# Optimization experiments

Hardware: AMD Instinct MI355X
Metric: run time of the kernel (lower is better)

Reference implementation:

```python
import jax, jax.numpy as jnp
import numpy as np

EMB = 1024
HEADS = 8
NUM_REL = 5
BS = 8
SLEN = 1024


def setup_inputs() -> dict:
    key = jax.random.key(0)
    ks = jax.random.split(key, 11)

    def lin(k, out_dim, in_dim):
        k1, k2 = jax.random.split(k)
        w = 0.02 * jax.random.normal(k1, (out_dim, in_dim), dtype=jnp.float32)
        b = 0.02 * jax.random.normal(k2, (out_dim,), dtype=jnp.float32)
        return w, b

    p = {}
    for i, pref in enumerate(["nq", "nk", "nv", "no", "tq", "tk", "tv", "to"]):
        w, b = lin(ks[i], EMB, EMB)
        p[pref + "_w"] = w
        p[pref + "_b"] = b
    tp_w, tp_b = lin(ks[8], NUM_REL, EMB)
    h_in = jax.random.normal(ks[9], (BS, SLEN, EMB), dtype=jnp.float32)
    word_mask = jnp.ones((BS, SLEN), dtype=bool)
    return {"h_in": h_in, "word_mask": word_mask, **p, "tp_w": tp_w, "tp_b": tp_b}


def _mha(x, mask, qw, qb, kw, kb, vw, vb, ow, ob):
    # Self-attention with key-padding mask; returns (output, attn_weights).
    bs, slen, dim = x.shape
    dh = dim // HEADS

    def split(t):  # [bs, slen, dim] -> [bs, h, slen, dh]
        return t.reshape(bs, slen, HEADS, dh).transpose(0, 2, 1, 3)

    q = split(x @ qw.T + qb) / jnp.sqrt(jnp.asarray(dh, x.dtype))
    k = split(x @ kw.T + kb)
    v = split(x @ vw.T + vb)
    scores = jnp.einsum('bhqd,bhkd->bhqk', q, k)
    scores = jnp.where(mask[:, None, None, :], scores, jnp.asarray(-1e9, x.dtype))
    w = jax.nn.softmax(scores, axis=-1)  # [bs, h, slen, slen]
    ctx = jnp.einsum('bhqk,bhkd->bhqd', w, v).transpose(0, 2, 1, 3).reshape(bs, slen, dim)
    return ctx @ ow.T + ob, w


def reference(h_in, word_mask, nq_w, nq_b, nk_w, nk_b, nv_w, nv_b, no_w, no_b,
              tq_w, tq_b, tk_w, tk_b, tv_w, tv_b, to_w, to_b, tp_w, tp_b):
    # Edge norms: sum attention weights over heads, then symmetrize.
    _, norm_w = _mha(h_in, word_mask, nq_w, nq_b, nk_w, nk_b, nv_w, nv_b, no_w, no_b)
    norm_w = norm_w.sum(axis=1)  # edge_norm_agg == 'sum' -> [bs, slen, slen]
    norms = norm_w + norm_w.transpose(0, 2, 1)

    # Edge types: second attention, project to relation logits, pairwise outer-sum.
    type_out, _ = _mha(h_in, word_mask, tq_w, tq_b, tk_w, tk_b, tv_w, tv_b, to_w, to_b)
    logits = type_out @ tp_w.T + tp_b  # [bs, slen, R]
    pair = logits[:, :, None, :] + logits[:, None, :, :]  # [bs, slen, slen, R]
    type_probs = jax.nn.softmax(pair, axis=-1)  # log_softmax(...).exp()
    return norms, type_probs
```

## Files before the change

kernel.cpp:

```cpp
#include <hip/hip_runtime.h>

using u16 = unsigned short;
typedef __bf16 bf16x8 __attribute__((ext_vector_type(8)));
typedef float  f32x4  __attribute__((ext_vector_type(4)));

__device__ __forceinline__ float b2f(u16 u){
  union { unsigned int i; float f; } v; v.i = ((unsigned int)u) << 16; return v.f;
}
__device__ __forceinline__ u16 f2b(float f){
  union { float f; unsigned int i; } v; v.f = f;
  unsigned int r = v.i + 0x7FFFu + ((v.i >> 16) & 1u);
  return (u16)(r >> 16);
}
__device__ __forceinline__ float waveMax(float v){
  #pragma unroll
  for (int o = 32; o > 0; o >>= 1) v = fmaxf(v, __shfl_xor(v, o, 64));
  return v;
}
__device__ __forceinline__ float waveSum(float v){
  #pragma unroll
  for (int o = 32; o > 0; o >>= 1) v += __shfl_xor(v, o, 64);
  return v;
}
__device__ __forceinline__ void async_cp16(const u16* g, u16* l){
  __builtin_amdgcn_global_load_lds((const __attribute__((address_space(1))) void*)g,
                                   (__attribute__((address_space(3))) void*)l, 16, 0, 0);
}

__global__ __launch_bounds__(256)
void cvt_f2b4(const float* __restrict__ s, u16* __restrict__ d, long long n4)
{
  long long i = (long long)blockIdx.x * 256 + threadIdx.x;
  long long st = (long long)gridDim.x * 256;
  for (; i < n4; i += st) {
    float4 v = ((const float4*)s)[i];
    ushort4 o; o.x = f2b(v.x); o.y = f2b(v.y); o.z = f2b(v.z); o.w = f2b(v.w);
    ((ushort4*)d)[i] = o;
  }
}

__global__ __launch_bounds__(256)
void bcat_k(const float* b0, const float* b1, const float* b2, const float* b3,
            const float* b4, float* __restrict__ dst)
{
  int t = blockIdx.x * 256 + threadIdx.x;
  const float* s = (t < 1024) ? b0 : (t < 2048) ? b1 : (t < 3072) ? b2 : (t < 4096) ? b3 : b4;
  dst[t] = s[t & 1023];
}

__global__ __launch_bounds__(256)
void fuse_w(const float* __restrict__ tow, const float* __restrict__ tob,
            const float* __restrict__ tpw, const float* __restrict__ tpb,
            float* __restrict__ Wc, float* __restrict__ bc)
{
  int t = blockIdx.x * 256 + threadIdx.x;
  int r = t >> 10, c = t & 1023;
  float acc = 0.f;
  for (int k = 0; k < 1024; k++) acc += tpw[r * 1024 + k] * tow[k * 1024 + c];
  Wc[t] = acc;
  if (t < 5) {
    float a = 0.f;
    for (int k = 0; k < 1024; k++) a += tpw[t * 1024 + k] * tob[k];
    bc[t] = a + tpb[t];
  }
}

template<int HAS_BIAS>
__global__ __launch_bounds__(256)
void gemm_bt(const u16* __restrict__ A, const u16* __restrict__ B,
             u16* __restrict__ C, const float* __restrict__ bias,
             int lda, int ldb, int ldc, int K,
             long long sAo, long long sAi, long long sBo, long long sBi,
             long long sCo, long long sCi, int zshift, int zmask, float alpha)
{
  int zo = (int)(blockIdx.z >> zshift), zi = (int)(blockIdx.z & zmask);
  A += zo * sAo + zi * sAi;
  B += zo * sBo + zi * sBi;
  long long coff = zo * sCo + zi * sCi;
  int m0 = blockIdx.y * 128, n0 = blockIdx.x * 128;

  __shared__ alignas(16) u16 sA[128 * 32];
  __shared__ alignas(16) u16 sB[128 * 32];

  int t = threadIdx.x;
  int lane = t & 63, wave = t >> 6;
  int quad = lane >> 4, l16 = lane & 15;
  int wm = (wave >> 1) << 6, wn = (wave & 1) << 6;
  int srow = t >> 2, scg = (t & 3) << 3;
  int wb = wave << 9;

  const u16* ga = A + (long long)(m0 + srow) * lda + scg;
  const u16* gb = B + (long long)(n0 + srow) * ldb + scg;

  f32x4 acc[4][4] = {};

  for (int k0 = 0; k0 < K; k0 += 32) {
    __syncthreads();
    async_cp16(ga + k0,                sA + wb);
    async_cp16(ga + 64ll * lda + k0,   sA + wb + 2048);
    async_cp16(gb + k0,                sB + wb);
    async_cp16(gb + 64ll * ldb + k0,   sB + wb + 2048);
    __syncthreads();

    bf16x8 af[4], bfr[4];
    #pragma unroll
    for (int mi = 0; mi < 4; mi++)
      af[mi] = *(const bf16x8*)(&sA[(wm + mi * 16 + l16) * 32 + quad * 8]);
    #pragma unroll
    for (int ni = 0; ni < 4; ni++)
      bfr[ni] = *(const bf16x8*)(&sB[(wn + ni * 16 + l16) * 32 + quad * 8]);
    #pragma unroll
    for (int mi = 0; mi < 4; mi++)
      #pragma unroll
      for (int ni = 0; ni < 4; ni++)
        acc[mi][ni] = __builtin_amdgcn_mfma_f32_16x16x32_bf16(af[mi], bfr[ni], acc[mi][ni], 0, 0, 0);
  }

  #pragma unroll
  for (int ni = 0; ni < 4; ni++) {
    int n = n0 + wn + ni * 16 + l16;
    float bv = 0.f;
    if (HAS_BIAS) bv = bias[n];
    #pragma unroll
    for (int mi = 0; mi < 4; mi++) {
      int mb = m0 + wm + mi * 16 + quad * 4;
      #pragma unroll
      for (int r = 0; r < 4; r++) {
        float v = alpha * (acc[mi][ni][r] + bv);
        C[coff + (long long)(mb + r) * ldc + n] = f2b(v);
      }
    }
  }
}

__global__ __launch_bounds__(256)
void norm_softmax_sum(const u16* __restrict__ sc, float* __restrict__ out)
{
  int i = blockIdx.x, b = blockIdx.y;
  int t = threadIdx.x;
  int wave = t >> 6;
  __shared__ float wm_[4], wsu[4];
  float acc[4] = {0.f, 0.f, 0.f, 0.f};

  for (int h = 0; h < 8; h++) {
    const u16* row = sc + (((long long)(b * 8 + h)) << 20) + ((long long)i << 10);
    float v[4];
    #pragma unroll
    for (int p = 0; p < 4; p++) v[p] = b2f(row[t + 256 * p]);
    float m = fmaxf(fmaxf(v[0], v[1]), fmaxf(v[2], v[3]));
    m = waveMax(m);
    if ((t & 63) == 0) wm_[wave] = m;
    __syncthreads();
    m = fmaxf(fmaxf(wm_[0], wm_[1]), fmaxf(wm_[2], wm_[3]));
    float e[4], s = 0.f;
    #pragma unroll
    for (int p = 0; p < 4; p++) { e[p] = __expf(v[p] - m); s += e[p]; }
    s = waveSum(s);
    if ((t & 63) == 0) wsu[wave] = s;
    __syncthreads();
    s = wsu[0] + wsu[1] + wsu[2] + wsu[3];
    float inv = 1.f / s;
    #pragma unroll
    for (int p = 0; p < 4; p++) acc[p] += e[p] * inv;
  }
  float* o = out + ((long long)b << 20) + ((long long)i << 10);
  #pragma unroll
  for (int p = 0; p < 4; p++) o[t + 256 * p] = acc[p];
}

__global__ __launch_bounds__(256)
void sym_inplace(float* __restrict__ nw)
{
  int tj = blockIdx.x, ti = blockIdx.y, b = blockIdx.z;
  if (tj < ti) return;
  float* base = nw + ((long long)b << 20);
  __shared__ float sij[64][65], sji[64][65];
  int t = threadIdx.x;
  #pragma unroll
  for (int p = 0; p < 16; p++) {
    int idx = p * 256 + t; int r = idx >> 6, c = idx & 63;
    sij[r][c] = base[(long long)(ti * 64 + r) * 1024 + tj * 64 + c];
    sji[r][c] = base[(long long)(tj * 64 + r) * 1024 + ti * 64 + c];
  }
  __syncthreads();
  #pragma unroll
  for (int p = 0; p < 16; p++) {
    int idx = p * 256 + t; int r = idx >> 6, c = idx & 63;
    base[(long long)(ti * 64 + r) * 1024 + tj * 64 + c] = sij[r][c] + sji[c][r];
    if (ti != tj)
      base[(long long)(tj * 64 + r) * 1024 + ti * 64 + c] = sji[r][c] + sij[c][r];
  }
}

__global__ __launch_bounds__(256)
void w5_k(const u16* __restrict__ proj, const float* __restrict__ Wc,
          float* __restrict__ w5)
{
  int jb = blockIdx.x, bh = blockIdx.y;
  int b = bh >> 3, h = bh & 7;
  int t = threadIdx.x;
  int j = jb * 256 + t;
  __shared__ float sWc[5][128];
  if (t < 128) {
    #pragma unroll
    for (int r = 0; r < 5; r++) sWc[r][t] = Wc[r * 1024 + h * 128 + t];
  }
  __syncthreads();
  const u16* vrow = proj + (long long)(b * 1024 + j) * 5120 + 4096 + h * 128;
  float acc[5] = {0.f, 0.f, 0.f, 0.f, 0.f};
  #pragma unroll
  for (int d0 = 0; d0 < 128; d0 += 8) {
    bf16x8 v = *(const bf16x8*)(vrow + d0);
    #pragma unroll
    for (int q = 0; q < 8; q++) {
      float f = (float)v[q];
      #pragma unroll
      for (int r = 0; r < 5; r++) acc[r] += f * sWc[r][d0 + q];
    }
  }
  #pragma unroll
  for (int r = 0; r < 5; r++) w5[(((long long)(bh * 5 + r)) << 10) + j] = acc[r];
}

__global__ __launch_bounds__(256)
void type_logits(const u16* __restrict__ sc, const float* __restrict__ w5,
                 const float* __restrict__ bc, float* __restrict__ lg)
{
  int b = blockIdx.y;
  int t = threadIdx.x;
  int wave = t >> 6, l = t & 63;
  int i = blockIdx.x * 4 + wave;
  __shared__ float sW5[5120];
  float acc[5] = {0.f, 0.f, 0.f, 0.f, 0.f};

  for (int h = 0; h < 8; h++) {
    const u16* row = sc + (((long long)(b * 8 + h)) << 20) + ((long long)i << 10);
    const float* wb = w5 + ((long long)(b * 8 + h)) * 5120;
    float v[16];
    #pragma unroll
    for (int k = 0; k < 16; k++) v[k] = b2f(row[l + 64 * k]);
    __syncthreads();
    #pragma unroll
    for (int p = 0; p < 20; p++) sW5[p * 256 + t] = wb[p * 256 + t];
    float m = v[0];
    #pragma unroll
    for (int k = 1; k < 16; k++) m = fmaxf(m, v[k]);
    m = waveMax(m);
    float e[16], s = 0.f;
    #pragma unroll
    for (int k = 0; k < 16; k++) { e[k] = __expf(v[k] - m); s += e[k]; }
    s = waveSum(s);
    float inv = 1.f / s;
    __syncthreads();
    #pragma unroll
    for (int r = 0; r < 5; r++) {
      float a = 0.f;
      #pragma unroll
      for (int k = 0; k < 16; k++) a += e[k] * sW5[r * 1024 + l + 64 * k];
      acc[r] += a * inv;
    }
  }
  #pragma unroll
  for (int r = 0; r < 5; r++) acc[r] = waveSum(acc[r]);
  if (l == 0) {
    #pragma unroll
    for (int r = 0; r < 5; r++) lg[(long long)(b * 1024 + i) * 5 + r] = acc[r] + bc[r];
  }
}

__global__ __launch_bounds__(256)
void pairwise_probs(const float* __restrict__ lg, float* __restrict__ out)
{
  int i = blockIdx.x, b = blockIdx.y;
  int t = threadIdx.x;
  __shared__ float sin_[5120];
  __shared__ float sout[5120];
  const float* lb = lg + (long long)b * 5120;
  #pragma unroll
  for (int p = 0; p < 20; p++) sin_[p * 256 + t] = lb[p * 256 + t];
  __syncthreads();
  float li[5];
  #pragma unroll
  for (int r = 0; r < 5; r++) li[r] = sin_[i * 5 + r];
  #pragma unroll
  for (int p = 0; p < 4; p++) {
    int j = t + 256 * p;
    float x[5]; float m = -1e30f;
    #pragma unroll
    for (int r = 0; r < 5; r++) { x[r] = li[r] + sin_[j * 5 + r]; m = fmaxf(m, x[r]); }
    float s = 0.f;
    #pragma unroll
    for (int r = 0; r < 5; r++) { x[r] = __expf(x[r] - m); s += x[r]; }
    float inv = 1.f / s;
    #pragma unroll
    for (int r = 0; r < 5; r++) sout[j * 5 + r] = x[r] * inv;
  }
  __syncthreads();
  float4* ob = (float4*)(out + ((long long)(b * 1024 + i)) * 5120);
  #pragma unroll
  for (int q = 0; q < 5; q++) ob[q * 256 + t] = ((const float4*)sout)[q * 256 + t];
}

extern "C" void kernel_launch(void* const* d_in, const int* in_sizes, int n_in,
                              void* d_out, int out_size, void* d_ws, size_t ws_size,
                              hipStream_t stream)
{
  const float* h_in = (const float*)d_in[0];
  const float* nq_w = (const float*)d_in[2];
  const float* nq_b = (const float*)d_in[3];
  const float* nk_w = (const float*)d_in[4];
  const float* nk_b = (const float*)d_in[5];
  const float* tq_w = (const float*)d_in[10];
  const float* tq_b = (const float*)d_in[11];
  const float* tk_w = (const float*)d_in[12];
  const float* tk_b = (const float*)d_in[13];
  const float* tv_w = (const float*)d_in[14];
  const float* tv_b = (const float*)d_in[15];
  const float* to_w = (const float*)d_in[16];
  const float* to_b = (const float*)d_in[17];
  const float* tp_w = (const float*)d_in[18];
  const float* tp_b = (const float*)d_in[19];

  char* ws = (char*)d_ws;
  u16*  hb   = (u16*)(ws);
  u16*  wcat = (u16*)(ws + (16ll  << 20));
  float* bcat= (float*)(ws + (26ll << 20));
  float* Wc  = (float*)(ws + (26ll << 20) + (512 << 10));
  float* bc  = (float*)(ws + (26ll << 20) + (768 << 10));
  float* lg  = (float*)(ws + (27ll << 20));
  u16*  proj = (u16*)(ws + (28ll  << 20));
  float* w5  = (float*)(ws + (108ll << 20));
  u16*  sc   = (u16*)(ws + (140ll << 20));

  float* out_norms = (float*)d_out;
  float* out_types = (float*)d_out + 8388608ll;

  const float qs = 0.08838834764831845f;
  dim3 blk(256);

  cvt_f2b4<<<dim3(2048), blk, 0, stream>>>(h_in, hb, 2097152ll);
  cvt_f2b4<<<dim3(512),  blk, 0, stream>>>(nq_w, wcat,              262144ll);
  cvt_f2b4<<<dim3(512),  blk, 0, stream>>>(nk_w, wcat + 1048576ll,  262144ll);
  cvt_f2b4<<<dim3(512),  blk, 0, stream>>>(tq_w, wcat + 2097152ll,  262144ll);
  cvt_f2b4<<<dim3(512),  blk, 0, stream>>>(tk_w, wcat + 3145728ll,  262144ll);
  cvt_f2b4<<<dim3(512),  blk, 0, stream>>>(tv_w, wcat + 4194304ll,  262144ll);
  bcat_k<<<dim3(20), blk, 0, stream>>>(nq_b, nk_b, tq_b, tk_b, tv_b, bcat);
  fuse_w<<<dim3(20), blk, 0, stream>>>(to_w, to_b, tp_w, tp_b, Wc, bc);

  gemm_bt<1><<<dim3(40,64,1), blk, 0, stream>>>(hb, wcat, proj, bcat,
      1024,1024,5120,1024, 0,0,0,0,0,0, 0,0, 1.f);

  w5_k<<<dim3(4,64), blk, 0, stream>>>(proj, Wc, w5);

  gemm_bt<0><<<dim3(8,8,64), blk, 0, stream>>>(proj, proj + 1024, sc, nullptr,
      5120,5120,1024,128, 5242880ll,128ll, 5242880ll,128ll, 8388608ll,1048576ll, 3,7, qs);
  norm_softmax_sum<<<dim3(1024,8), blk, 0, stream>>>(sc, out_norms);
  sym_inplace<<<dim3(16,16,8), blk, 0, stream>>>(out_norms);

  gemm_bt<0><<<dim3(8,8,64), blk, 0, stream>>>(proj + 2048, proj + 3072, sc, nullptr,
      5120,5120,1024,128, 5242880ll,128ll, 5242880ll,128ll, 8388608ll,1048576ll, 3,7, qs);
  type_logits<<<dim3(256,8), blk, 0, stream>>>(sc, w5, bc, lg);
  pairwise_probs<<<dim3(1024,8), blk, 0, stream>>>(lg, out_types);
}
```

Before: 741.8 us.

## Fuse norm QK^T with softmax-sum and fold V projection into relation weights

New measurement: 789.5 us. 1.06x slower.

```diff
diff --git a/kernel.cpp b/kernel.cpp
--- a/kernel.cpp
+++ b/kernel.cpp
@@ -41,10 +41,10 @@
 
 __global__ __launch_bounds__(256)
 void bcat_k(const float* b0, const float* b1, const float* b2, const float* b3,
-            const float* b4, float* __restrict__ dst)
+            float* __restrict__ dst)
 {
   int t = blockIdx.x * 256 + threadIdx.x;
-  const float* s = (t < 1024) ? b0 : (t < 2048) ? b1 : (t < 3072) ? b2 : (t < 4096) ? b3 : b4;
+  const float* s = (t < 1024) ? b0 : (t < 2048) ? b1 : (t < 3072) ? b2 : b3;
   dst[t] = s[t & 1023];
 }
 
@@ -65,7 +65,32 @@
   }
 }
 
-template<int HAS_BIAS>
+__global__ __launch_bounds__(256)
+void fuse_wf(const float* __restrict__ tvw, const float* __restrict__ tvb,
+             const float* __restrict__ Wc, u16* __restrict__ WF,
+             float* __restrict__ bias5)
+{
+  int idx = blockIdx.x * 256 + threadIdx.x;
+  int n = idx >> 10, k = idx & 1023;
+  float acc = 0.f;
+  if (n < 40) {
+    int h = n / 5, r = n - h * 5;
+    const float* wcr = Wc + r * 1024 + h * 128;
+    const float* tw = tvw + (h * 128) * 1024 + k;
+    for (int d = 0; d < 128; d++) acc += wcr[d] * tw[d * 1024];
+  }
+  WF[idx] = f2b(acc);
+  if (k == 0) {
+    float a = 0.f;
+    if (n < 40) {
+      int h = n / 5, r = n - h * 5;
+      for (int d = 0; d < 128; d++) a += Wc[r * 1024 + h * 128 + d] * tvb[h * 128 + d];
+    }
+    bias5[n] = a;
+  }
+}
+
+template<int HAS_BIAS, int OUT_F32>
 __global__ __launch_bounds__(256)
 void gemm_bt(const u16* __restrict__ A, const u16* __restrict__ B,
              u16* __restrict__ C, const float* __restrict__ bias,
@@ -127,45 +152,114 @@
       #pragma unroll
       for (int r = 0; r < 4; r++) {
         float v = alpha * (acc[mi][ni][r] + bv);
-        C[coff + (long long)(mb + r) * ldc + n] = f2b(v);
+        if (OUT_F32) ((float*)C)[coff + (long long)(mb + r) * ldc + n] = v;
+        else         C[coff + (long long)(mb + r) * ldc + n] = f2b(v);
       }
     }
   }
 }
 
-__global__ __launch_bounds__(256)
-void norm_softmax_sum(const u16* __restrict__ sc, float* __restrict__ out)
-{
-  int i = blockIdx.x, b = blockIdx.y;
+__global__ __launch_bounds__(512)
+void norm_fused(const u16* __restrict__ proj, float* __restrict__ out)
+{
+  int b = blockIdx.y, i0 = blockIdx.x * 32;
   int t = threadIdx.x;
-  int wave = t >> 6;
-  __shared__ float wm_[4], wsu[4];
-  float acc[4] = {0.f, 0.f, 0.f, 0.f};
+  int lane = t & 63, wave = t >> 6;
+  int quad = lane >> 4, l16 = lane & 15;
+  int wm = (wave >> 2) << 4;
+  int wn = (wave & 3) << 4;
+  int r0 = t >> 4, g = t & 15;
+
+  __shared__ alignas(16) u16 sQ[2][32 * 128];
+  __shared__ alignas(16) u16 sK[2][64 * 128];
+  __shared__ alignas(16) u16 sS[32 * 1044];
+
+  const long long ldp = 4096;
+  const u16* pb = proj + (long long)(b * 1024) * ldp;
+  int srow = t >> 4;
+  int scol = (t & 15) << 3;
+  const float qs = 0.08838834764831845f;
+
+  float acc[16][4];
+  #pragma unroll
+  for (int k = 0; k < 16; k++)
+    #pragma unroll
+    for (int j = 0; j < 4; j++) acc[k][j] = 0.f;
+
+  auto stageQ = [&](int h, int buf){
+    async_cp16(pb + (long long)(i0 + srow) * ldp + h * 128 + scol,
+               &sQ[buf][wave << 9]);
+  };
+  auto stageK = [&](int h, int jt, int buf){
+    const u16* gbase = pb + 1024 + h * 128 + scol;
+    #pragma unroll
+    for (int c = 0; c < 2; c++)
+      async_cp16(gbase + (long long)(jt * 64 + c * 32 + srow) * ldp,
+                 &sK[buf][c * 4096 + (wave << 9)]);
+  };
+
+  int qb = 0, kb = 0;
+  stageQ(0, 0);
+  stageK(0, 0, 0);
+  __syncthreads();
 
   for (int h = 0; h < 8; h++) {
-    const u16* row = sc + (((long long)(b * 8 + h)) << 20) + ((long long)i << 10);
-    float v[4];
-    #pragma unroll
-    for (int p = 0; p < 4; p++) v[p] = b2f(row[t + 256 * p]);
-    float m = fmaxf(fmaxf(v[0], v[1]), fmaxf(v[2], v[3]));
-    m = waveMax(m);
-    if ((t & 63) == 0) wm_[wave] = m;
+    for (int jt = 0; jt < 16; jt++) {
+      if (jt < 15)      stageK(h, jt + 1, kb ^ 1);
+      else if (h < 7) { stageK(h + 1, 0, kb ^ 1); stageQ(h + 1, qb ^ 1); }
+
+      f32x4 accs = {};
+      #pragma unroll
+      for (int kk = 0; kk < 4; kk++) {
+        bf16x8 af  = *(const bf16x8*)(&sQ[qb][(wm + l16) * 128 + kk * 32 + quad * 8]);
+        bf16x8 bf_ = *(const bf16x8*)(&sK[kb][(wn + l16) * 128 + kk * 32 + quad * 8]);
+        accs = __builtin_amdgcn_mfma_f32_16x16x32_bf16(af, bf_, accs, 0, 0, 0);
+      }
+      int jg = jt * 64 + wn + l16;
+      #pragma unroll
+      for (int rr = 0; rr < 4; rr++)
+        sS[(wm + quad * 4 + rr) * 1044 + jg] = f2b(qs * accs[rr]);
+      __syncthreads();
+      kb ^= 1;
+    }
+
+    const u16* sr = sS + r0 * 1044 + g * 4;
+    float m = -1e30f;
+    #pragma unroll
+    for (int k = 0; k < 16; k++) {
+      ushort4 u = *(const ushort4*)(sr + k * 64);
+      m = fmaxf(m, fmaxf(fmaxf(b2f(u.x), b2f(u.y)), fmaxf(b2f(u.z), b2f(u.w))));
+    }
+    #pragma unroll
+    for (int o = 1; o < 16; o <<= 1) m = fmaxf(m, __shfl_xor(m, o, 64));
+    float s = 0.f;
+    #pragma unroll
+    for (int k = 0; k < 16; k++) {
+      ushort4 u = *(const ushort4*)(sr + k * 64);
+      s += __expf(b2f(u.x) - m) + __expf(b2f(u.y) - m)
+         + __expf(b2f(u.z) - m) + __expf(b2f(u.w) - m);
+    }
+    #pragma unroll
+    for (int o = 1; o < 16; o <<= 1) s += __shfl_xor(s, o, 64);
+    float inv = 1.f / s;
+    #pragma unroll
+    for (int k = 0; k < 16; k++) {
+      ushort4 u = *(const ushort4*)(sr + k * 64);
+      acc[k][0] += __expf(b2f(u.x) - m) * inv;
+      acc[k][1] += __expf(b2f(u.y) - m) * inv;
+      acc[k][2] += __expf(b2f(u.z) - m) * inv;
+      acc[k][3] += __expf(b2f(u.w) - m) * inv;
+    }
     __syncthreads();
-    m = fmaxf(fmaxf(wm_[0], wm_[1]), fmaxf(wm_[2], wm_[3]));
-    float e[4], s = 0.f;
-    #pragma unroll
-    for (int p = 0; p < 4; p++) { e[p] = __expf(v[p] - m); s += e[p]; }
-    s = waveSum(s);
-    if ((t & 63) == 0) wsu[wave] = s;
-    __syncthreads();
-    s = wsu[0] + wsu[1] + wsu[2] + wsu[3];
-    float inv = 1.f / s;
-    #pragma unroll
-    for (int p = 0; p < 4; p++) acc[p] += e[p] * inv;
-  }
-  float* o = out + ((long long)b << 20) + ((long long)i << 10);
-  #pragma unroll
-  for (int p = 0; p < 4; p++) o[t + 256 * p] = acc[p];
+    qb ^= 1;
+  }
+
+  float* orow = out + ((long long)b << 20) + ((long long)(i0 + r0) << 10) + g * 4;
+  #pragma unroll
+  for (int k = 0; k < 16; k++) {
+    float4 o4 = make_float4(acc[k][0], acc[k][1], acc[k][2], acc[k][3]);
+    *(float4*)(orow + k * 64) = o4;
+  }
 }
 
 __global__ __launch_bounds__(256)
@@ -193,33 +287,14 @@
 }
 
 __global__ __launch_bounds__(256)
-void w5_k(const u16* __restrict__ proj, const float* __restrict__ Wc,
-          float* __restrict__ w5)
-{
-  int jb = blockIdx.x, bh = blockIdx.y;
-  int b = bh >> 3, h = bh & 7;
-  int t = threadIdx.x;
-  int j = jb * 256 + t;
-  __shared__ float sWc[5][128];
-  if (t < 128) {
-    #pragma unroll
-    for (int r = 0; r < 5; r++) sWc[r][t] = Wc[r * 1024 + h * 128 + t];
-  }
-  __syncthreads();
-  const u16* vrow = proj + (long long)(b * 1024 + j) * 5120 + 4096 + h * 128;
-  float acc[5] = {0.f, 0.f, 0.f, 0.f, 0.f};
-  #pragma unroll
-  for (int d0 = 0; d0 < 128; d0 += 8) {
-    bf16x8 v = *(const bf16x8*)(vrow + d0);
-    #pragma unroll
-    for (int q = 0; q < 8; q++) {
-      float f = (float)v[q];
-      #pragma unroll
-      for (int r = 0; r < 5; r++) acc[r] += f * sWc[r][d0 + q];
-    }
-  }
-  #pragma unroll
-  for (int r = 0; r < 5; r++) w5[(((long long)(bh * 5 + r)) << 10) + j] = acc[r];
+void w5_tr(const float* __restrict__ w5b, float* __restrict__ w5)
+{
+  int bh = blockIdx.y, b = bh >> 3, h = bh & 7;
+  int j = blockIdx.x * 256 + threadIdx.x;
+  const float* src = w5b + (long long)(b * 1024 + j) * 128 + h * 5;
+  float* dst = w5 + (long long)bh * 5120 + j;
+  #pragma unroll
+  for (int r = 0; r < 5; r++) dst[r * 1024] = src[r];
 }
 
 __global__ __launch_bounds__(256)
@@ -322,15 +397,18 @@
   const float* tp_b = (const float*)d_in[19];
 
   char* ws = (char*)d_ws;
-  u16*  hb   = (u16*)(ws);
-  u16*  wcat = (u16*)(ws + (16ll  << 20));
-  float* bcat= (float*)(ws + (26ll << 20));
-  float* Wc  = (float*)(ws + (26ll << 20) + (512 << 10));
-  float* bc  = (float*)(ws + (26ll << 20) + (768 << 10));
-  float* lg  = (float*)(ws + (27ll << 20));
-  u16*  proj = (u16*)(ws + (28ll  << 20));
-  float* w5  = (float*)(ws + (108ll << 20));
-  u16*  sc   = (u16*)(ws + (140ll << 20));
+  u16*   hb    = (u16*)(ws);
+  u16*   wcat  = (u16*)(ws + (16ll << 20));
+  float* bcat  = (float*)(ws + (24ll << 20));
+  float* Wc    = (float*)(ws + (24ll << 20) + (64 << 10));
+  float* bc    = (float*)(ws + (24ll << 20) + (128 << 10));
+  float* bias5 = (float*)(ws + (24ll << 20) + (192 << 10));
+  u16*   WF    = (u16*)(ws + (24ll << 20) + (256 << 10));
+  float* lg    = (float*)(ws + (25ll << 20));
+  float* w5b   = (float*)(ws + (26ll << 20));
+  float* w5    = (float*)(ws + (30ll << 20));
+  u16*   proj  = (u16*)(ws + (32ll << 20));
+  u16*   sc    = (u16*)(ws + (96ll << 20));
 
   float* out_norms = (float*)d_out;
   float* out_types = (float*)d_out + 8388608ll;
@@ -343,22 +421,22 @@
   cvt_f2b4<<<dim3(512),  blk, 0, stream>>>(nk_w, wcat + 1048576ll,  262144ll);
   cvt_f2b4<<<dim3(512),  blk, 0, stream>>>(tq_w, wcat + 2097152ll,  262144ll);
   cvt_f2b4<<<dim3(512),  blk, 0, stream>>>(tk_w, wcat + 3145728ll,  262144ll);
-  cvt_f2b4<<<dim3(512),  blk, 0, stream>>>(tv_w, wcat + 4194304ll,  262144ll);
-  bcat_k<<<dim3(20), blk, 0, stream>>>(nq_b, nk_b, tq_b, tk_b, tv_b, bcat);
+  bcat_k<<<dim3(16), blk, 0, stream>>>(nq_b, nk_b, tq_b, tk_b, bcat);
   fuse_w<<<dim3(20), blk, 0, stream>>>(to_w, to_b, tp_w, tp_b, Wc, bc);
-
-  gemm_bt<1><<<dim3(40,64,1), blk, 0, stream>>>(hb, wcat, proj, bcat,
-      1024,1024,5120,1024, 0,0,0,0,0,0, 0,0, 1.f);
-
-  w5_k<<<dim3(4,64), blk, 0, stream>>>(proj, Wc, w5);
-
-  gemm_bt<0><<<dim3(8,8,64), blk, 0, stream>>>(proj, proj + 1024, sc, nullptr,
-      5120,5120,1024,128, 5242880ll,128ll, 5242880ll,128ll, 8388608ll,1048576ll, 3,7, qs);
-  norm_softmax_sum<<<dim3(1024,8), blk, 0, stream>>>(sc, out_norms);
+  fuse_wf<<<dim3(512), blk, 0, stream>>>(tv_w, tv_b, Wc, WF, bias5);
+
+  gemm_bt<1,0><<<dim3(32,64,1), blk, 0, stream>>>(hb, wcat, proj, bcat,
+      1024,1024,4096,1024, 0,0,0,0,0,0, 0,0, 1.f);
+
+  gemm_bt<1,1><<<dim3(1,64,1), blk, 0, stream>>>(hb, WF, (u16*)w5b, bias5,
+      1024,1024,128,1024, 0,0,0,0,0,0, 0,0, 1.f);
+  w5_tr<<<dim3(4,64), blk, 0, stream>>>(w5b, w5);
+
+  norm_fused<<<dim3(32,8), dim3(512), 0, stream>>>(proj, out_norms);
   sym_inplace<<<dim3(16,16,8), blk, 0, stream>>>(out_norms);
 
-  gemm_bt<0><<<dim3(8,8,64), blk, 0, stream>>>(proj + 2048, proj + 3072, sc, nullptr,
-      5120,5120,1024,128, 5242880ll,128ll, 5242880ll,128ll, 8388608ll,1048576ll, 3,7, qs);
+  gemm_bt<0,0><<<dim3(8,8,64), blk, 0, stream>>>(proj + 2048, proj + 3072, sc, nullptr,
+      4096,4096,1024,128, 4194304ll,128ll, 4194304ll,128ll, 8388608ll,1048576ll, 3,7, qs);
   type_logits<<<dim3(256,8), blk, 0, stream>>>(sc, w5, bc, lg);
   pairwise_probs<<<dim3(1024,8), blk, 0, stream>>>(lg, out_types);
 }
```
